# Kernel optimization log

Hardware: AMD Instinct MI355X
Metric: run time of the kernel (lower is better)

The kernel has to match this reference:

```python
import jax, jax.numpy as jnp
import numpy as np

B, T, D = 64, 512, 256
UNITS, MEM = 512, 64


def _glorot(key, shape):
    fan_in, fan_out = shape
    lim = np.sqrt(6.0 / (fan_in + fan_out))
    return jax.random.uniform(key, shape, jnp.float32, -lim, lim)


def setup_inputs() -> dict:
    key = jax.random.key(0)
    ks = jax.random.split(key, 12)
    return {
        "x": jax.random.normal(ks[0], (B, T, D), jnp.float32),
        "Wi": _glorot(ks[1], (D, UNITS)), "Ui": _glorot(ks[2], (UNITS, UNITS)), "bi": jnp.zeros((UNITS,), jnp.float32),
        "Wf": _glorot(ks[3], (D, UNITS)), "Uf": _glorot(ks[4], (UNITS, UNITS)), "bf": jnp.ones((UNITS,), jnp.float32),
        "Wo": _glorot(ks[5], (D, UNITS)), "Uo": _glorot(ks[6], (UNITS, UNITS)), "bo": jnp.zeros((UNITS,), jnp.float32),
        "Wc": _glorot(ks[7], (D, UNITS)), "Uc": _glorot(ks[8], (UNITS, UNITS)), "bc": jnp.zeros((UNITS,), jnp.float32),
        "Wm": _glorot(ks[9], (D, UNITS)),
        "We": _glorot(ks[10], (D, MEM)), "Ue": _glorot(ks[11], (UNITS, MEM)), "be": jnp.zeros((MEM,), jnp.float32),
    }


def _clip(v):
    return jnp.clip(v, -10.0, 10.0)


def reference(x, Wi, Ui, bi, Wf, Uf, bf, Wo, Uo, bo, Wc, Uc, bc, Wm, We, Ue, be):
    def step(carry, xt):
        h, mem = carry  # h: [B,U], mem: [B,MEM,U]
        xt = _clip(xt)
        i = jax.nn.sigmoid(_clip(xt @ Wi + h @ Ui + bi))
        f = jax.nn.sigmoid(_clip(xt @ Wf + h @ Uf + bf))
        o = jax.nn.sigmoid(_clip(xt @ Wo + h @ Uo + bo))
        c_tilde = jnp.tanh(_clip(xt @ Wc + h @ Uc + bc))
        e = jax.nn.softmax(_clip(xt @ We + h @ Ue + be), axis=-1)  # [B,MEM]
        memory_attention = jnp.sum(mem * e[:, :, None], axis=1)  # [B,U]
        c = f * (memory_attention + xt @ Wm) + i * c_tilde
        h_new = o * jnp.tanh(c)
        mem_new = jnp.concatenate([c[:, None, :], mem[:, :-1, :]], axis=1)
        return (h_new, mem_new), h_new

    h0 = jnp.zeros((x.shape[0], UNITS), x.dtype)
    m0 = jnp.zeros((x.shape[0], MEM, UNITS), x.dtype)
    (_, _), hs = jax.lax.scan(step, (h0, m0), jnp.swapaxes(x, 0, 1))
    return jnp.swapaxes(hs, 0, 1)  # [B,T,U]
```

## Files before the change

kernel.cpp:

```cpp
#include <hip/hip_runtime.h>
#include <hip/hip_bf16.h>

typedef unsigned short ushortT;
typedef __attribute__((ext_vector_type(8))) short bf16x8;
typedef __attribute__((ext_vector_type(4))) float f32x4;
typedef __attribute__((ext_vector_type(4))) int i32x4;

#define B_SZ 64
#define T_SZ 512
#define D_SZ 256
#define U_SZ 512
#define M_SZ 64

__device__ __forceinline__ ushortT f2b(float f) {
    __hip_bfloat16 h = __float2bfloat16(f);
    union { __hip_bfloat16 h; ushortT u; } c; c.h = h; return c.u;
}
__device__ __forceinline__ float clip10(float v) {
    return fminf(fmaxf(v, -10.f), 10.f);
}
__device__ __forceinline__ float tanh_fast(float z) {
    float e = __expf(2.f * z);
    return 1.f - 2.f / (e + 1.f);
}
__device__ __forceinline__ float sigm_fast(float z) {
    return 1.f / (1.f + __expf(-z));
}

__global__ void prep_xb_k(const float* __restrict__ x, ushortT* __restrict__ xb) {
    const int n4 = (B_SZ * T_SZ * D_SZ) / 4;
    for (int i = blockIdx.x * blockDim.x + threadIdx.x; i < n4; i += gridDim.x * blockDim.x) {
        float4 v = ((const float4*)x)[i];
        ushort4 o;
        o.x = f2b(clip10(v.x));
        o.y = f2b(clip10(v.y));
        o.z = f2b(clip10(v.z));
        o.w = f2b(clip10(v.w));
        ((ushort4*)xb)[i] = o;
    }
}

__global__ void prep_uw_k(const float* __restrict__ Ui, const float* __restrict__ Uf,
                          const float* __restrict__ Uo, const float* __restrict__ Uc,
                          const float* __restrict__ Ue,
                          const float* __restrict__ Wi, const float* __restrict__ Wf,
                          const float* __restrict__ Wo, const float* __restrict__ Wc,
                          const float* __restrict__ We, const float* __restrict__ Wm,
                          ushortT* __restrict__ UslT, ushortT* __restrict__ WslT) {
    const int NU = 2112 * 512;
    const int NW = 2624 * 256;
    for (int i = blockIdx.x * blockDim.x + threadIdx.x; i < NU + NW; i += gridDim.x * blockDim.x) {
        if (i < NU) {
            int c = i >> 9, k = i & 511;
            float v;
            if (c < 2048) {
                int g = c >> 9, u = c & 511;
                const float* U = (g == 0) ? Ui : (g == 1) ? Uf : (g == 2) ? Uo : Uc;
                v = U[k * 512 + u];
            } else {
                v = Ue[k * 64 + (c - 2048)];
            }
            UslT[i] = f2b(v);
        } else {
            int j = i - NU;
            int c = j >> 8, k = j & 255;
            float v;
            if (c < 2048) {
                int g = c >> 9, u = c & 511;
                const float* W = (g == 0) ? Wi : (g == 1) ? Wf : (g == 2) ? Wo : Wc;
                v = W[k * 512 + u];
            } else if (c < 2112) {
                v = We[k * 64 + (c - 2048)];
            } else {
                v = Wm[k * 512 + (c - 2112)];
            }
            WslT[j] = f2b(v);
        }
    }
}

#define MEMF_PB 1096
#define MEMF_ROW 68

__global__ __launch_bounds__(256, 1) void xlstm_rec(
    const ushortT* __restrict__ xb,
    const ushortT* __restrict__ UslT,
    const ushortT* __restrict__ WslT,
    const float* __restrict__ bi_p, const float* __restrict__ bf_p,
    const float* __restrict__ bo_p, const float* __restrict__ bc_p,
    const float* __restrict__ be_p,
    unsigned* __restrict__ Hbuf32,
    unsigned* __restrict__ Hmir,
    float* __restrict__ out)
{
    const int bid = blockIdx.x, tid = threadIdx.x;
    const int grp = bid & 7, rank = bid >> 3;
    const int wave = tid >> 6, lane = tid & 63;
    const int b0 = grp << 3;
    const int u0 = rank << 4;

    __shared__ float memF[8 * MEMF_PB];
    __shared__ float g_lds[4][8][16];
    __shared__ float e_lds[8][68];
    __shared__ float w_lds[8][72];
    __shared__ float zm_lds[8][16];
    __shared__ ushortT hLb[8][520];

    for (int i = tid; i < 8 * MEMF_PB; i += 256) memF[i] = 0.f;

    int cols[2];
    float biasv[2];
#pragma unroll
    for (int nt = 0; nt < 2; ++nt) {
        int j = wave * 32 + nt * 16 + (lane & 15);
        if (j < 64) {
            int g = j >> 4, u = u0 + (j & 15);
            cols[nt] = g * 512 + u;
            biasv[nt] = (g == 0) ? bi_p[u] : (g == 1) ? bf_p[u] : (g == 2) ? bo_p[u] : bc_p[u];
        } else {
            cols[nt] = 2048 + (j - 64);
            biasv[nt] = be_p[j - 64];
        }
    }
    const int koct = (lane >> 4) * 8;
    bf16x8 B1[2][8], B2[2][16], B1m[8];
#pragma unroll
    for (int nt = 0; nt < 2; ++nt) {
        const ushortT* bw = WslT + cols[nt] * 256;
#pragma unroll
        for (int kt = 0; kt < 8; ++kt)
            B1[nt][kt] = *(const bf16x8*)(bw + kt * 32 + koct);
        const ushortT* bu = UslT + cols[nt] * 512;
#pragma unroll
        for (int kt = 0; kt < 16; ++kt)
            B2[nt][kt] = *(const bf16x8*)(bu + kt * 32 + koct);
    }
    if (wave == 1) {
        const ushortT* bm = WslT + (2112 + u0 + (lane & 15)) * 256;
#pragma unroll
        for (int kt = 0; kt < 8; ++kt)
            B1m[kt] = *(const bf16x8*)(bm + kt * 32 + koct);
    }

    const int arow = lane & 7;
    const bool is_pw = (tid >= 64 && tid < 192);
    const int pb = (tid - 64) >> 4;
    const int pu = (tid - 64) & 15;
    const int prow = 2 * wave + (lane >> 5);
    const int pcol = (lane & 31) * 16;

    __syncthreads();

    for (int t = 0; t < T_SZ; ++t) {
        const int par = t & 1, wpar = (t + 1) & 1;
        const unsigned T16 = ((unsigned)t) << 16;

        i32x4 a1f[8];
        {
            const ushortT* xrow = xb + ((b0 + arow) * T_SZ + t) * D_SZ + koct;
#pragma unroll
            for (int kt = 0; kt < 8; ++kt)
                asm volatile("global_load_dwordx4 %0, %1, off"
                             : "=v"(a1f[kt]) : "v"(xrow + kt * 32) : "memory");
        }

        const unsigned* msrc = Hmir + (par << 15) + (b0 + prow) * 512 + pcol;
        const unsigned* hsrc = Hbuf32 + (par << 15) + (b0 + prow) * 512 + pcol;
        i32x4 g0, g1, g2, g3;
        asm volatile("global_load_dwordx4 %0, %4, off sc0\n\t"
                     "global_load_dwordx4 %1, %4, off offset:16 sc0\n\t"
                     "global_load_dwordx4 %2, %4, off offset:32 sc0\n\t"
                     "global_load_dwordx4 %3, %4, off offset:48 sc0"
                     : "=v"(g0), "=v"(g1), "=v"(g2), "=v"(g3)
                     : "v"(msrc) : "memory");
        asm volatile("s_waitcnt vmcnt(4)"
                     : "+v"(a1f[0]), "+v"(a1f[1]), "+v"(a1f[2]), "+v"(a1f[3]),
                       "+v"(a1f[4]), "+v"(a1f[5]), "+v"(a1f[6]), "+v"(a1f[7])
                     :: "memory");
        __builtin_amdgcn_sched_barrier(0);

        f32x4 acc0 = {0.f, 0.f, 0.f, 0.f}, acc1 = {0.f, 0.f, 0.f, 0.f};
        f32x4 acc2 = {0.f, 0.f, 0.f, 0.f};
#pragma unroll
        for (int kt = 0; kt < 8; ++kt) {
            bf16x8 a = __builtin_bit_cast(bf16x8, a1f[kt]);
            acc0 = __builtin_amdgcn_mfma_f32_16x16x32_bf16(a, B1[0][kt], acc0, 0, 0, 0);
            acc1 = __builtin_amdgcn_mfma_f32_16x16x32_bf16(a, B1[1][kt], acc1, 0, 0, 0);
        }
        if (wave == 1) {
#pragma unroll
            for (int kt = 0; kt < 8; ++kt) {
                bf16x8 a = __builtin_bit_cast(bf16x8, a1f[kt]);
                acc2 = __builtin_amdgcn_mfma_f32_16x16x32_bf16(a, B1m[kt], acc2, 0, 0, 0);
            }
        }

        {
            unsigned it = 0;
            while (true) {
                asm volatile("s_waitcnt vmcnt(0)"
                             : "+v"(g0), "+v"(g1), "+v"(g2), "+v"(g3) :: "memory");
                unsigned d = (((unsigned)g0[0] ^ T16) | ((unsigned)g0[1] ^ T16)) |
                             (((unsigned)g0[2] ^ T16) | ((unsigned)g0[3] ^ T16));
                d |= (((unsigned)g1[0] ^ T16) | ((unsigned)g1[1] ^ T16)) |
                     (((unsigned)g1[2] ^ T16) | ((unsigned)g1[3] ^ T16));
                d |= (((unsigned)g2[0] ^ T16) | ((unsigned)g2[1] ^ T16)) |
                     (((unsigned)g2[2] ^ T16) | ((unsigned)g2[3] ^ T16));
                d |= (((unsigned)g3[0] ^ T16) | ((unsigned)g3[1] ^ T16)) |
                     (((unsigned)g3[2] ^ T16) | ((unsigned)g3[3] ^ T16));
                if (__all((d & 0xFFFF0000u) == 0u)) break;
                if ((it & 1u) == 0u) {
                    asm volatile("global_load_dwordx4 %0, %4, off sc0 sc1\n\t"
                                 "global_load_dwordx4 %1, %4, off offset:16 sc0 sc1\n\t"
                                 "global_load_dwordx4 %2, %4, off offset:32 sc0 sc1\n\t"
                                 "global_load_dwordx4 %3, %4, off offset:48 sc0 sc1"
                                 : "=v"(g0), "=v"(g1), "=v"(g2), "=v"(g3)
                                 : "v"(hsrc) : "memory");
                } else {
                    asm volatile("global_load_dwordx4 %0, %4, off sc0\n\t"
                                 "global_load_dwordx4 %1, %4, off offset:16 sc0\n\t"
                                 "global_load_dwordx4 %2, %4, off offset:32 sc0\n\t"
                                 "global_load_dwordx4 %3, %4, off offset:48 sc0"
                                 : "=v"(g0), "=v"(g1), "=v"(g2), "=v"(g3)
                                 : "v"(msrc) : "memory");
                }
                ++it;
            }
        }
        __builtin_amdgcn_sched_barrier(0);

        {
            unsigned p0 = ((unsigned)g0[0] & 0xFFFFu) | ((unsigned)g0[1] << 16);
            unsigned p1 = ((unsigned)g0[2] & 0xFFFFu) | ((unsigned)g0[3] << 16);
            unsigned p2 = ((unsigned)g1[0] & 0xFFFFu) | ((unsigned)g1[1] << 16);
            unsigned p3 = ((unsigned)g1[2] & 0xFFFFu) | ((unsigned)g1[3] << 16);
            unsigned p4 = ((unsigned)g2[0] & 0xFFFFu) | ((unsigned)g2[1] << 16);
            unsigned p5 = ((unsigned)g2[2] & 0xFFFFu) | ((unsigned)g2[3] << 16);
            unsigned p6 = ((unsigned)g3[0] & 0xFFFFu) | ((unsigned)g3[1] << 16);
            unsigned p7 = ((unsigned)g3[2] & 0xFFFFu) | ((unsigned)g3[3] << 16);
            i32x4 P0 = {(int)p0, (int)p1, (int)p2, (int)p3};
            i32x4 P1 = {(int)p4, (int)p5, (int)p6, (int)p7};
            *(i32x4*)&hLb[prow][pcol] = P0;
            *(i32x4*)&hLb[prow][pcol + 8] = P1;
        }
        __syncthreads();

#pragma unroll
        for (int kt = 0; kt < 16; ++kt) {
            bf16x8 a = *(const bf16x8*)&hLb[arow][kt * 32 + koct];
            acc0 = __builtin_amdgcn_mfma_f32_16x16x32_bf16(a, B2[0][kt], acc0, 0, 0, 0);
            acc1 = __builtin_amdgcn_mfma_f32_16x16x32_bf16(a, B2[1][kt], acc1, 0, 0, 0);
        }

        if (lane < 32) {
#pragma unroll
            for (int nt = 0; nt < 2; ++nt) {
                int j = wave * 32 + nt * 16 + (lane & 15);
                f32x4 a = nt ? acc1 : acc0;
#pragma unroll
                for (int i = 0; i < 4; ++i) {
                    int b = ((lane >> 4) << 2) + i;
                    float z = clip10(a[i] + biasv[nt]);
                    if (j < 64) {
                        int g = j >> 4;
                        g_lds[g][b][j & 15] = (g == 3) ? tanh_fast(z) : sigm_fast(z);
                    } else {
                        e_lds[b][j - 64] = z;
                    }
                }
            }
            if (wave == 1) {
#pragma unroll
                for (int i = 0; i < 4; ++i)
                    zm_lds[((lane >> 4) << 2) + i][lane & 15] = acc2[i];
            }
        }
        __syncthreads();

        if (is_pw) {
            const int base = pu * 4;
            const int k0 = t - 1 - base;
            float wv0 = __expf(e_lds[pb][(unsigned)(k0) & 63]);
            float wv1 = __expf(e_lds[pb][(unsigned)(k0 - 1) & 63]);
            float wv2 = __expf(e_lds[pb][(unsigned)(k0 - 2) & 63]);
            float wv3 = __expf(e_lds[pb][(unsigned)(k0 - 3) & 63]);
            float ssum = (wv0 + wv1) + (wv2 + wv3);
#pragma unroll
            for (int d = 1; d < 16; d <<= 1) ssum += __shfl_xor(ssum, d);
            float4 wq = {wv0, wv1, wv2, wv3};
            *(float4*)&w_lds[pb][base] = wq;
            asm volatile("" ::: "memory");
            float attn = 0.f;
            const float4* wr = (const float4*)&w_lds[pb][0];
            const float4* mr = (const float4*)&memF[pb * MEMF_PB + pu * MEMF_ROW];
#pragma unroll
            for (int p4i = 0; p4i < 16; ++p4i) {
                float4 w4 = wr[p4i], m4 = mr[p4i];
                attn = fmaf(w4.x, m4.x, attn);
                attn = fmaf(w4.y, m4.y, attn);
                attn = fmaf(w4.z, m4.z, attn);
                attn = fmaf(w4.w, m4.w, attn);
            }
            attn /= ssum;
            float ig = g_lds[0][pb][pu];
            float fg = g_lds[1][pb][pu];
            float og = g_lds[2][pb][pu];
            float ct = g_lds[3][pb][pu];
            float c = fg * (attn + zm_lds[pb][pu]) + ig * ct;
            float h = og * tanh_fast(c);
            unsigned tagval = (((unsigned)(t + 1)) << 16) | (unsigned)f2b(h);
            const unsigned off = (unsigned)((wpar << 15) + (b0 + pb) * 512 + u0 + pu);
            asm volatile("global_store_dword %0, %1, off sc0"
                         :: "v"(Hmir + off), "v"(tagval) : "memory");
            asm volatile("global_store_dword %0, %1, off sc0 sc1"
                         :: "v"(Hbuf32 + off), "v"(tagval) : "memory");
            const float* oaddr = out + ((b0 + pb) * T_SZ + t) * U_SZ + u0 + pu;
            asm volatile("global_store_dword %0, %1, off"
                         :: "v"(oaddr), "v"(h) : "memory");
            memF[pb * MEMF_PB + pu * MEMF_ROW + (t & 63)] = c;
        }
    }
}

extern "C" void kernel_launch(void* const* d_in, const int* in_sizes, int n_in,
                              void* d_out, int out_size, void* d_ws, size_t ws_size,
                              hipStream_t stream) {
    const float* x  = (const float*)d_in[0];
    const float* Wi = (const float*)d_in[1];
    const float* Ui = (const float*)d_in[2];
    const float* bi = (const float*)d_in[3];
    const float* Wf = (const float*)d_in[4];
    const float* Uf = (const float*)d_in[5];
    const float* bf = (const float*)d_in[6];
    const float* Wo = (const float*)d_in[7];
    const float* Uo = (const float*)d_in[8];
    const float* bo = (const float*)d_in[9];
    const float* Wc = (const float*)d_in[10];
    const float* Uc = (const float*)d_in[11];
    const float* bc = (const float*)d_in[12];
    const float* Wm = (const float*)d_in[13];
    const float* We = (const float*)d_in[14];
    const float* Ue = (const float*)d_in[15];
    const float* be = (const float*)d_in[16];

    char* ws = (char*)d_ws;
    const size_t off_xb    = 0;
    const size_t off_uslt  = off_xb + (size_t)B_SZ * T_SZ * D_SZ * 2;
    const size_t off_wslt  = off_uslt + (size_t)2112 * 512 * 2;
    const size_t off_hbuf  = off_wslt + (size_t)2624 * 256 * 2;
    const size_t off_hmir  = off_hbuf + 262144;
    ushortT* xb       = (ushortT*)(ws + off_xb);
    ushortT* UslT     = (ushortT*)(ws + off_uslt);
    ushortT* WslT     = (ushortT*)(ws + off_wslt);
    unsigned* Hbuf32  = (unsigned*)(ws + off_hbuf);
    unsigned* Hmir    = (unsigned*)(ws + off_hmir);
    float* out = (float*)d_out;

    (void)hipMemsetAsync(ws + off_hbuf, 0, 524288, stream);

    prep_xb_k<<<2048, 256, 0, stream>>>(x, xb);
    prep_uw_k<<<2048, 256, 0, stream>>>(Ui, Uf, Uo, Uc, Ue, Wi, Wf, Wo, Wc, We, Wm,
                                        UslT, WslT);

    xlstm_rec<<<dim3(256), dim3(256), 0, stream>>>(
        xb, UslT, WslT, bi, bf, bo, bc, be, Hbuf32, Hmir, out);
}
```

Before: 1.657 ms.

## Stream tagged h directly into MFMA A-operands, removing LDS staging and barrier

```diff
diff --git a/kernel.cpp b/kernel.cpp
--- a/kernel.cpp
+++ b/kernel.cpp
@@ -82,6 +82,62 @@
 #define MEMF_PB 1096
 #define MEMF_ROW 68
 
+#define ISSUE_MIR(R, P)                                                        \
+    asm volatile("global_load_dwordx4 %0, %8, off sc0\n\t"                     \
+                 "global_load_dwordx4 %1, %8, off offset:16 sc0\n\t"           \
+                 "global_load_dwordx4 %2, %8, off offset:128 sc0\n\t"          \
+                 "global_load_dwordx4 %3, %8, off offset:144 sc0\n\t"          \
+                 "global_load_dwordx4 %4, %8, off offset:256 sc0\n\t"          \
+                 "global_load_dwordx4 %5, %8, off offset:272 sc0\n\t"          \
+                 "global_load_dwordx4 %6, %8, off offset:384 sc0\n\t"          \
+                 "global_load_dwordx4 %7, %8, off offset:400 sc0"              \
+                 : "=v"(R[0]), "=v"(R[1]), "=v"(R[2]), "=v"(R[3]),             \
+                   "=v"(R[4]), "=v"(R[5]), "=v"(R[6]), "=v"(R[7])              \
+                 : "v"(P) : "memory")
+#define ISSUE_LLC(R, P)                                                        \
+    asm volatile("global_load_dwordx4 %0, %8, off sc0 sc1\n\t"                 \
+                 "global_load_dwordx4 %1, %8, off offset:16 sc0 sc1\n\t"       \
+                 "global_load_dwordx4 %2, %8, off offset:128 sc0 sc1\n\t"      \
+                 "global_load_dwordx4 %3, %8, off offset:144 sc0 sc1\n\t"      \
+                 "global_load_dwordx4 %4, %8, off offset:256 sc0 sc1\n\t"      \
+                 "global_load_dwordx4 %5, %8, off offset:272 sc0 sc1\n\t"      \
+                 "global_load_dwordx4 %6, %8, off offset:384 sc0 sc1\n\t"      \
+                 "global_load_dwordx4 %7, %8, off offset:400 sc0 sc1"          \
+                 : "=v"(R[0]), "=v"(R[1]), "=v"(R[2]), "=v"(R[3]),             \
+                   "=v"(R[4]), "=v"(R[5]), "=v"(R[6]), "=v"(R[7])              \
+                 : "v"(P) : "memory")
+#define WAITQ(N, R)                                                            \
+    asm volatile("s_waitcnt vmcnt(" #N ")"                                     \
+                 : "+v"(R[0]), "+v"(R[1]), "+v"(R[2]), "+v"(R[3]),             \
+                   "+v"(R[4]), "+v"(R[5]), "+v"(R[6]), "+v"(R[7])              \
+                 :: "memory")
+#define TAG4(RR) (((unsigned)RR[0] ^ T16) | ((unsigned)RR[1] ^ T16) |          \
+                  ((unsigned)RR[2] ^ T16) | ((unsigned)RR[3] ^ T16))
+#define DO_KT(R0, R1, KT)                                                      \
+    {                                                                          \
+        unsigned l0 = ((unsigned)R0[0] & 0xFFFFu) | ((unsigned)R0[1] << 16);   \
+        unsigned l1 = ((unsigned)R0[2] & 0xFFFFu) | ((unsigned)R0[3] << 16);   \
+        unsigned l2 = ((unsigned)R1[0] & 0xFFFFu) | ((unsigned)R1[1] << 16);   \
+        unsigned l3 = ((unsigned)R1[2] & 0xFFFFu) | ((unsigned)R1[3] << 16);   \
+        i32x4 P = {(int)l0, (int)l1, (int)l2, (int)l3};                        \
+        bf16x8 a = __builtin_bit_cast(bf16x8, P);                              \
+        acc0 = __builtin_amdgcn_mfma_f32_16x16x32_bf16(a, B2[0][KT], acc0, 0, 0, 0); \
+        acc1 = __builtin_amdgcn_mfma_f32_16x16x32_bf16(a, B2[1][KT], acc1, 0, 0, 0); \
+    }
+#define VALIDATE_Q(R, MQ, LQ)                                                  \
+    {                                                                          \
+        unsigned att = 0;                                                      \
+        while (true) {                                                         \
+            unsigned d = TAG4(R[0]) | TAG4(R[1]) | TAG4(R[2]) | TAG4(R[3]) |   \
+                         TAG4(R[4]) | TAG4(R[5]) | TAG4(R[6]) | TAG4(R[7]);    \
+            if (__all((d & 0xFFFF0000u) == 0u)) break;                         \
+            slow = true;                                                       \
+            if (att % 3u == 2u) { ISSUE_LLC(R, LQ); } else { ISSUE_MIR(R, MQ); } \
+            WAITQ(0, R);                                                       \
+            ++att;                                                             \
+        }                                                                      \
+    }
+
 __global__ __launch_bounds__(256, 1) void xlstm_rec(
     const ushortT* __restrict__ xb,
     const ushortT* __restrict__ UslT,
@@ -104,7 +160,6 @@
     __shared__ float e_lds[8][68];
     __shared__ float w_lds[8][72];
     __shared__ float zm_lds[8][16];
-    __shared__ ushortT hLb[8][520];
 
     for (int i = tid; i < 8 * MEMF_PB; i += 256) memF[i] = 0.f;
 
@@ -146,8 +201,6 @@
     const bool is_pw = (tid >= 64 && tid < 192);
     const int pb = (tid - 64) >> 4;
     const int pu = (tid - 64) & 15;
-    const int prow = 2 * wave + (lane >> 5);
-    const int pcol = (lane & 31) * 16;
 
     __syncthreads();
 
@@ -164,16 +217,12 @@
                              : "=v"(a1f[kt]) : "v"(xrow + kt * 32) : "memory");
         }
 
-        const unsigned* msrc = Hmir + (par << 15) + (b0 + prow) * 512 + pcol;
-        const unsigned* hsrc = Hbuf32 + (par << 15) + (b0 + prow) * 512 + pcol;
-        i32x4 g0, g1, g2, g3;
-        asm volatile("global_load_dwordx4 %0, %4, off sc0\n\t"
-                     "global_load_dwordx4 %1, %4, off offset:16 sc0\n\t"
-                     "global_load_dwordx4 %2, %4, off offset:32 sc0\n\t"
-                     "global_load_dwordx4 %3, %4, off offset:48 sc0"
-                     : "=v"(g0), "=v"(g1), "=v"(g2), "=v"(g3)
-                     : "v"(msrc) : "memory");
-        asm volatile("s_waitcnt vmcnt(4)"
+        const unsigned* mbase = Hmir + (par << 15) + (b0 + arow) * 512 + koct;
+        const unsigned* lbase = Hbuf32 + (par << 15) + (b0 + arow) * 512 + koct;
+        i32x4 RA[8], RB[8];
+        ISSUE_MIR(RA, mbase);
+        ISSUE_MIR(RB, mbase + 128);
+        asm volatile("s_waitcnt vmcnt(16)"
                      : "+v"(a1f[0]), "+v"(a1f[1]), "+v"(a1f[2]), "+v"(a1f[3]),
                        "+v"(a1f[4]), "+v"(a1f[5]), "+v"(a1f[6]), "+v"(a1f[7])
                      :: "memory");
@@ -195,62 +244,29 @@
             }
         }
 
-        {
-            unsigned it = 0;
-            while (true) {
-                asm volatile("s_waitcnt vmcnt(0)"
-                             : "+v"(g0), "+v"(g1), "+v"(g2), "+v"(g3) :: "memory");
-                unsigned d = (((unsigned)g0[0] ^ T16) | ((unsigned)g0[1] ^ T16)) |
-                             (((unsigned)g0[2] ^ T16) | ((unsigned)g0[3] ^ T16));
-                d |= (((unsigned)g1[0] ^ T16) | ((unsigned)g1[1] ^ T16)) |
-                     (((unsigned)g1[2] ^ T16) | ((unsigned)g1[3] ^ T16));
-                d |= (((unsigned)g2[0] ^ T16) | ((unsigned)g2[1] ^ T16)) |
-                     (((unsigned)g2[2] ^ T16) | ((unsigned)g2[3] ^ T16));
-                d |= (((unsigned)g3[0] ^ T16) | ((unsigned)g3[1] ^ T16)) |
-                     (((unsigned)g3[2] ^ T16) | ((unsigned)g3[3] ^ T16));
-                if (__all((d & 0xFFFF0000u) == 0u)) break;
-                if ((it & 1u) == 0u) {
-                    asm volatile("global_load_dwordx4 %0, %4, off sc0 sc1\n\t"
-                                 "global_load_dwordx4 %1, %4, off offset:16 sc0 sc1\n\t"
-                                 "global_load_dwordx4 %2, %4, off offset:32 sc0 sc1\n\t"
-                                 "global_load_dwordx4 %3, %4, off offset:48 sc0 sc1"
-                                 : "=v"(g0), "=v"(g1), "=v"(g2), "=v"(g3)
-                                 : "v"(hsrc) : "memory");
-                } else {
-                    asm volatile("global_load_dwordx4 %0, %4, off sc0\n\t"
-                                 "global_load_dwordx4 %1, %4, off offset:16 sc0\n\t"
-                                 "global_load_dwordx4 %2, %4, off offset:32 sc0\n\t"
-                                 "global_load_dwordx4 %3, %4, off offset:48 sc0"
-                                 : "=v"(g0), "=v"(g1), "=v"(g2), "=v"(g3)
-                                 : "v"(msrc) : "memory");
-                }
-                ++it;
-            }
-        }
-        __builtin_amdgcn_sched_barrier(0);
-
-        {
-            unsigned p0 = ((unsigned)g0[0] & 0xFFFFu) | ((unsigned)g0[1] << 16);
-            unsigned p1 = ((unsigned)g0[2] & 0xFFFFu) | ((unsigned)g0[3] << 16);
-            unsigned p2 = ((unsigned)g1[0] & 0xFFFFu) | ((unsigned)g1[1] << 16);
-            unsigned p3 = ((unsigned)g1[2] & 0xFFFFu) | ((unsigned)g1[3] << 16);
-            unsigned p4 = ((unsigned)g2[0] & 0xFFFFu) | ((unsigned)g2[1] << 16);
-            unsigned p5 = ((unsigned)g2[2] & 0xFFFFu) | ((unsigned)g2[3] << 16);
-            unsigned p6 = ((unsigned)g3[0] & 0xFFFFu) | ((unsigned)g3[1] << 16);
-            unsigned p7 = ((unsigned)g3[2] & 0xFFFFu) | ((unsigned)g3[3] << 16);
-            i32x4 P0 = {(int)p0, (int)p1, (int)p2, (int)p3};
-            i32x4 P1 = {(int)p4, (int)p5, (int)p6, (int)p7};
-            *(i32x4*)&hLb[prow][pcol] = P0;
-            *(i32x4*)&hLb[prow][pcol + 8] = P1;
-        }
-        __syncthreads();
-
-#pragma unroll
-        for (int kt = 0; kt < 16; ++kt) {
-            bf16x8 a = *(const bf16x8*)&hLb[arow][kt * 32 + koct];
-            acc0 = __builtin_amdgcn_mfma_f32_16x16x32_bf16(a, B2[0][kt], acc0, 0, 0, 0);
-            acc1 = __builtin_amdgcn_mfma_f32_16x16x32_bf16(a, B2[1][kt], acc1, 0, 0, 0);
-        }
+        bool slow = false;
+        if (!slow) { WAITQ(8, RA); } else { WAITQ(0, RA); }
+        __builtin_amdgcn_sched_barrier(0);
+        VALIDATE_Q(RA, mbase, lbase);
+        DO_KT(RA[0], RA[1], 0) DO_KT(RA[2], RA[3], 1)
+        DO_KT(RA[4], RA[5], 2) DO_KT(RA[6], RA[7], 3)
+        ISSUE_MIR(RA, mbase + 256);
+        if (!slow) { WAITQ(8, RB); } else { WAITQ(0, RB); }
+        __builtin_amdgcn_sched_barrier(0);
+        VALIDATE_Q(RB, mbase + 128, lbase + 128);
+        DO_KT(RB[0], RB[1], 4) DO_KT(RB[2], RB[3], 5)
+        DO_KT(RB[4], RB[5], 6) DO_KT(RB[6], RB[7], 7)
+        ISSUE_MIR(RB, mbase + 384);
+        if (!slow) { WAITQ(8, RA); } else { WAITQ(0, RA); }
+        __builtin_amdgcn_sched_barrier(0);
+        VALIDATE_Q(RA, mbase + 256, lbase + 256);
+        DO_KT(RA[0], RA[1], 8)  DO_KT(RA[2], RA[3], 9)
+        DO_KT(RA[4], RA[5], 10) DO_KT(RA[6], RA[7], 11)
+        WAITQ(0, RB);
+        __builtin_amdgcn_sched_barrier(0);
+        VALIDATE_Q(RB, mbase + 384, lbase + 384);
+        DO_KT(RB[0], RB[1], 12) DO_KT(RB[2], RB[3], 13)
+        DO_KT(RB[4], RB[5], 14) DO_KT(RB[6], RB[7], 15)
 
         if (lane < 32) {
 #pragma unroll
```

Result: slower. 4.654 ms (+180.9%).
